# Kernel tuning notes

Hardware: AMD Instinct MI355X
Metric: run time of the kernel (lower is better)

## Reference

```python
import jax, jax.numpy as jnp
import numpy as np

N = 524288       # total nodes
B = 1024         # number of graphs
EMB = 128        # emb_size


def setup_inputs() -> dict:
    key = jax.random.key(0)
    ks = jax.random.split(key, 9)
    x = jax.random.normal(ks[0], (N, EMB), dtype=jnp.float32)
    g_prev = jax.random.normal(ks[1], (B, EMB), dtype=jnp.float32)
    batch_idx = jnp.sort(jax.random.randint(ks[2], (N,), 0, B)).astype(jnp.int32)
    # gate_nn: Linear(emb, 1); value nn: Linear(emb, emb); mlp: Linear(2*emb, emb)
    Wg = jax.random.normal(ks[3], (EMB, 1), dtype=jnp.float32) / np.sqrt(EMB)
    bg = jnp.zeros((1,), dtype=jnp.float32)
    Wv = jax.random.normal(ks[4], (EMB, EMB), dtype=jnp.float32) / np.sqrt(EMB)
    bv = jnp.zeros((EMB,), dtype=jnp.float32)
    Wm = jax.random.normal(ks[5], (2 * EMB, EMB), dtype=jnp.float32) / np.sqrt(2 * EMB)
    bm = jnp.zeros((EMB,), dtype=jnp.float32)
    return {"x": x, "g_prev": g_prev, "batch_idx": batch_idx,
            "Wg": Wg, "bg": bg, "Wv": Wv, "bv": bv, "Wm": Wm, "bm": bm}


def reference(x, g_prev, batch_idx, Wg, bg, Wv, bv, Wm, bm):
    nb = g_prev.shape[0]
    # AttentionalAggregation: gate = gate_nn(x) [N,1], value = nn(x) [N,emb]
    gate = (x @ Wg + bg)[:, 0]                                   # [N]
    val = x @ Wv + bv                                            # [N, emb]
    # segment softmax over batch_idx (numerically stable)
    seg_max = jax.ops.segment_max(gate, batch_idx, num_segments=nb)
    seg_max = jnp.where(jnp.isfinite(seg_max), seg_max, 0.0)
    e = jnp.exp(gate - jax.lax.stop_gradient(seg_max)[batch_idx])  # [N]
    denom = jax.ops.segment_sum(e, batch_idx, num_segments=nb)     # [B]
    alpha = e / denom[batch_idx]                                   # [N]
    # weighted scatter-sum -> pooled graph embedding [B, emb]
    g = jax.ops.segment_sum(val * alpha[:, None], batch_idx, num_segments=nb)
    # residual MLP: g_prev + leaky_relu(Linear(concat([g, g_prev])))
    h = jnp.concatenate([g, g_prev], axis=-1) @ Wm + bm            # [B, emb]
    return g_prev + jax.nn.leaky_relu(h, negative_slope=0.01)
```

## Files before the change

kernel.cpp:

```cpp
#include <hip/hip_runtime.h>
#include <math.h>

#define EMB 128

__global__ void seg_start_kernel(const int* __restrict__ bidx,
                                 int* __restrict__ start, int n, int nb) {
    int i = blockIdx.x * blockDim.x + threadIdx.x;
    if (i >= n) return;
    int bi = bidx[i];
    int bp = (i == 0) ? -1 : bidx[i - 1];
    for (int b = bp + 1; b <= bi; ++b) start[b] = i;
    if (i == n - 1) {
        for (int b = bi + 1; b <= nb; ++b) start[b] = n;
    }
}

__launch_bounds__(256, 4)
__global__ void pool_kernel(const float* __restrict__ x,
                            const float* __restrict__ g_prev,
                            const int* __restrict__ seg_start,
                            const float* __restrict__ Wg,
                            const float* __restrict__ bg,
                            const float* __restrict__ Wv,
                            const float* __restrict__ bv,
                            const float* __restrict__ Wm,
                            const float* __restrict__ bm,
                            float* __restrict__ out) {
    const int b    = blockIdx.x;
    const int tid  = threadIdx.x;
    const int lane = tid & 63;
    const int warp = tid >> 6;
    const int half = lane >> 5;
    const int sub  = lane & 31;
    const int h    = warp * 2 + half;

    __shared__ float sh_m[8];
    __shared__ float sh_d[8];
    __shared__ float sh_s[8][128];
    __shared__ float sh_t[128];
    __shared__ float sh_g[128];
    __shared__ float sh_gp[128];
    __shared__ int   sh_se[2];

    if (tid == 0) { sh_se[0] = seg_start[b]; sh_se[1] = seg_start[b + 1]; }
    __syncthreads();
    const int start = sh_se[0];
    const int end   = sh_se[1];

    float4 wg  = *reinterpret_cast<const float4*>(Wg + 4 * sub);
    float  bg0 = bg[0];

    float  m = -INFINITY;
    float  d = 0.0f;
    float4 s = make_float4(0.f, 0.f, 0.f, 0.f);

    int r = start + h;
    float4 xc = make_float4(0.f, 0.f, 0.f, 0.f);
    if (r < end)
        xc = *reinterpret_cast<const float4*>(x + (size_t)r * EMB + 4 * sub);

    for (; r < end; r += 8) {
        float4 xn = make_float4(0.f, 0.f, 0.f, 0.f);
        int rn = r + 8;
        if (rn < end)
            xn = *reinterpret_cast<const float4*>(x + (size_t)rn * EMB + 4 * sub);

        float p = xc.x * wg.x + xc.y * wg.y + xc.z * wg.z + xc.w * wg.w;
        #pragma unroll
        for (int off = 16; off >= 1; off >>= 1) p += __shfl_xor(p, off);
        float gate = p + bg0;

        float mnew = fmaxf(m, gate);
        float corr = __expf(m - mnew);
        float e    = __expf(gate - mnew);
        d   = d * corr + e;
        s.x = s.x * corr + e * xc.x;
        s.y = s.y * corr + e * xc.y;
        s.z = s.z * corr + e * xc.z;
        s.w = s.w * corr + e * xc.w;
        m   = mnew;
        xc  = xn;
    }

    *reinterpret_cast<float4*>(&sh_s[h][4 * sub]) = s;
    if (sub == 0) { sh_m[h] = m; sh_d[h] = d; }
    __syncthreads();

    if (tid < 128) {
        float M = -INFINITY;
        #pragma unroll
        for (int i = 0; i < 8; ++i) M = fmaxf(M, sh_m[i]);
        float ts = 0.f, ds = 0.f;
        #pragma unroll
        for (int i = 0; i < 8; ++i) {
            float mi = sh_m[i];
            float w  = (mi == -INFINITY) ? 0.0f : __expf(mi - M);
            ts += w * sh_s[i][tid];
            ds += w * sh_d[i];
        }
        sh_t[tid] = (start < end) ? (ts / ds) : 0.0f;
    }
    __syncthreads();

    if (tid < 128) {
        float acc = 0.0f;
        if (start < end) {
            acc = bv[tid];
            for (int k = 0; k < 128; ++k)
                acc += sh_t[k] * Wv[k * 128 + tid];
        }
        sh_g[tid]  = acc;
        sh_gp[tid] = g_prev[(size_t)b * EMB + tid];
    }
    __syncthreads();

    if (tid < 128) {
        float hacc = bm[tid];
        for (int k = 0; k < 128; ++k)
            hacc += sh_g[k] * Wm[k * 128 + tid];
        for (int k = 0; k < 128; ++k)
            hacc += sh_gp[k] * Wm[(128 + k) * 128 + tid];
        float gp = sh_gp[tid];
        out[(size_t)b * EMB + tid] = gp + (hacc > 0.f ? hacc : 0.01f * hacc);
    }
}

extern "C" void kernel_launch(void* const* d_in, const int* in_sizes, int n_in,
                              void* d_out, int out_size, void* d_ws, size_t ws_size,
                              hipStream_t stream) {
    const float* x      = (const float*)d_in[0];
    const float* g_prev = (const float*)d_in[1];
    const int*   bidx   = (const int*)d_in[2];
    const float* Wg     = (const float*)d_in[3];
    const float* bg     = (const float*)d_in[4];
    const float* Wv     = (const float*)d_in[5];
    const float* bv     = (const float*)d_in[6];
    const float* Wm     = (const float*)d_in[7];
    const float* bm     = (const float*)d_in[8];
    float* out = (float*)d_out;

    const int N = in_sizes[0] / EMB;
    const int B = in_sizes[1] / EMB;

    int* seg_start = (int*)d_ws;

    seg_start_kernel<<<(N + 255) / 256, 256, 0, stream>>>(bidx, seg_start, N, B);
    pool_kernel<<<B, 256, 0, stream>>>(x, g_prev, seg_start,
                                       Wg, bg, Wv, bv, Wm, bm, out);
}
```

Before: 388.6 us.

## Process four rows per half-wave per iteration and split epilogue GEMVs across all threads

The streaming loop now has each 32-lane half-wave load and process four consecutive rows per iteration, with the next four prefetched. This raises memory-level parallelism and batches the shuffle reductions and online-softmax rescaling over four rows. The per-graph GEMVs (Wv and the two halves of Wm) are now split across all 256 threads, each summing half of K, with partial sums combined through shared memory. The cost is higher register pressure under launch bounds of 4 blocks per SM and extra barriers in the epilogue.

Measured after the change: 387.2 us. About the same (-0.3%).

```diff
diff --git a/kernel.cpp b/kernel.cpp
--- a/kernel.cpp
+++ b/kernel.cpp
@@ -40,6 +40,7 @@
     __shared__ float sh_t[128];
     __shared__ float sh_g[128];
     __shared__ float sh_gp[128];
+    __shared__ float sh_p[2][128];
     __shared__ int   sh_se[2];
 
     if (tid == 0) { sh_se[0] = seg_start[b]; sh_se[1] = seg_start[b + 1]; }
@@ -54,32 +55,60 @@
     float  d = 0.0f;
     float4 s = make_float4(0.f, 0.f, 0.f, 0.f);
 
-    int r = start + h;
-    float4 xc = make_float4(0.f, 0.f, 0.f, 0.f);
-    if (r < end)
-        xc = *reinterpret_cast<const float4*>(x + (size_t)r * EMB + 4 * sub);
+    const float4 zero4 = make_float4(0.f, 0.f, 0.f, 0.f);
 
-    for (; r < end; r += 8) {
-        float4 xn = make_float4(0.f, 0.f, 0.f, 0.f);
-        int rn = r + 8;
-        if (rn < end)
-            xn = *reinterpret_cast<const float4*>(x + (size_t)rn * EMB + 4 * sub);
+    int r0 = start + h * 4;
+    float4 xc0 = zero4, xc1 = zero4, xc2 = zero4, xc3 = zero4;
+    if (r0 + 0 < end) xc0 = *reinterpret_cast<const float4*>(x + (size_t)(r0 + 0) * EMB + 4 * sub);
+    if (r0 + 1 < end) xc1 = *reinterpret_cast<const float4*>(x + (size_t)(r0 + 1) * EMB + 4 * sub);
+    if (r0 + 2 < end) xc2 = *reinterpret_cast<const float4*>(x + (size_t)(r0 + 2) * EMB + 4 * sub);
+    if (r0 + 3 < end) xc3 = *reinterpret_cast<const float4*>(x + (size_t)(r0 + 3) * EMB + 4 * sub);
 
-        float p = xc.x * wg.x + xc.y * wg.y + xc.z * wg.z + xc.w * wg.w;
+    for (; r0 < end; ) {
+        const int rn = r0 + 32;
+        float4 xn0 = zero4, xn1 = zero4, xn2 = zero4, xn3 = zero4;
+        if (rn < end) {
+            xn0 = *reinterpret_cast<const float4*>(x + (size_t)(rn + 0) * EMB + 4 * sub);
+            if (rn + 1 < end) xn1 = *reinterpret_cast<const float4*>(x + (size_t)(rn + 1) * EMB + 4 * sub);
+            if (rn + 2 < end) xn2 = *reinterpret_cast<const float4*>(x + (size_t)(rn + 2) * EMB + 4 * sub);
+            if (rn + 3 < end) xn3 = *reinterpret_cast<const float4*>(x + (size_t)(rn + 3) * EMB + 4 * sub);
+        }
+
+        float p0 = xc0.x * wg.x + xc0.y * wg.y + xc0.z * wg.z + xc0.w * wg.w;
+        float p1 = xc1.x * wg.x + xc1.y * wg.y + xc1.z * wg.z + xc1.w * wg.w;
+        float p2 = xc2.x * wg.x + xc2.y * wg.y + xc2.z * wg.z + xc2.w * wg.w;
+        float p3 = xc3.x * wg.x + xc3.y * wg.y + xc3.z * wg.z + xc3.w * wg.w;
+
         #pragma unroll
-        for (int off = 16; off >= 1; off >>= 1) p += __shfl_xor(p, off);
-        float gate = p + bg0;
+        for (int off = 16; off >= 1; off >>= 1) {
+            p0 += __shfl_xor(p0, off);
+            p1 += __shfl_xor(p1, off);
+            p2 += __shfl_xor(p2, off);
+            p3 += __shfl_xor(p3, off);
+        }
 
-        float mnew = fmaxf(m, gate);
+        float g0 = p0 + bg0;
+        float g1 = (r0 + 1 < end) ? (p1 + bg0) : -INFINITY;
+        float g2 = (r0 + 2 < end) ? (p2 + bg0) : -INFINITY;
+        float g3 = (r0 + 3 < end) ? (p3 + bg0) : -INFINITY;
+
+        float mb   = fmaxf(fmaxf(g0, g1), fmaxf(g2, g3));
+        float mnew = fmaxf(m, mb);
         float corr = __expf(m - mnew);
-        float e    = __expf(gate - mnew);
-        d   = d * corr + e;
-        s.x = s.x * corr + e * xc.x;
-        s.y = s.y * corr + e * xc.y;
-        s.z = s.z * corr + e * xc.z;
-        s.w = s.w * corr + e * xc.w;
+        float e0 = __expf(g0 - mnew);
+        float e1 = __expf(g1 - mnew);
+        float e2 = __expf(g2 - mnew);
+        float e3 = __expf(g3 - mnew);
+
+        d   = d * corr + (e0 + e1 + e2 + e3);
+        s.x = s.x * corr + e0 * xc0.x + e1 * xc1.x + e2 * xc2.x + e3 * xc3.x;
+        s.y = s.y * corr + e0 * xc0.y + e1 * xc1.y + e2 * xc2.y + e3 * xc3.y;
+        s.z = s.z * corr + e0 * xc0.z + e1 * xc1.z + e2 * xc2.z + e3 * xc3.z;
+        s.w = s.w * corr + e0 * xc0.w + e1 * xc1.w + e2 * xc2.w + e3 * xc3.w;
         m   = mnew;
-        xc  = xn;
+
+        xc0 = xn0; xc1 = xn1; xc2 = xn2; xc3 = xn3;
+        r0  = rn;
     }
 
     *reinterpret_cast<float4*>(&sh_s[h][4 * sub]) = s;
@@ -98,29 +127,41 @@
             ts += w * sh_s[i][tid];
             ds += w * sh_d[i];
         }
-        sh_t[tid] = (start < end) ? (ts / ds) : 0.0f;
-    }
-    __syncthreads();
-
-    if (tid < 128) {
-        float acc = 0.0f;
-        if (start < end) {
-            acc = bv[tid];
-            for (int k = 0; k < 128; ++k)
-                acc += sh_t[k] * Wv[k * 128 + tid];
-        }
-        sh_g[tid]  = acc;
+        sh_t[tid]  = (start < end) ? (ts / ds) : 0.0f;
         sh_gp[tid] = g_prev[(size_t)b * EMB + tid];
     }
     __syncthreads();
 
+    {
+        const int col = tid & 127;
+        const int kh  = tid >> 7;
+        float acc = 0.0f;
+        #pragma unroll 4
+        for (int k = kh * 64; k < kh * 64 + 64; ++k)
+            acc += sh_t[k] * Wv[k * 128 + col];
+        sh_p[kh][col] = acc;
+    }
+    __syncthreads();
     if (tid < 128) {
-        float hacc = bm[tid];
+        sh_g[tid] = (start < end) ? (sh_p[0][tid] + sh_p[1][tid] + bv[tid]) : 0.0f;
+    }
+    __syncthreads();
+
+    {
+        const int col = tid & 127;
+        const int kh  = tid >> 7;
+        const float* src = (kh == 0) ? sh_g : sh_gp;
+        const float* wmp = Wm + (size_t)kh * 128 * 128;
+        float acc = 0.0f;
+        #pragma unroll 4
         for (int k = 0; k < 128; ++k)
-            hacc += sh_g[k] * Wm[k * 128 + tid];
-        for (int k = 0; k < 128; ++k)
-            hacc += sh_gp[k] * Wm[(128 + k) * 128 + tid];
-        float gp = sh_gp[tid];
+            acc += src[k] * wmp[k * 128 + col];
+        sh_p[kh][col] = acc;
+    }
+    __syncthreads();
+    if (tid < 128) {
+        float hacc = sh_p[0][tid] + sh_p[1][tid] + bm[tid];
+        float gp   = sh_gp[tid];
         out[(size_t)b * EMB + tid] = gp + (hacc > 0.f ? hacc : 0.01f * hacc);
     }
 }
```
